# Optimization experiments

Measured on AMD Instinct MI355X. Metric: run time of the kernel, lower is better.

Reference implementation:

```python
import jax, jax.numpy as jnp
import numpy as np

B = 64
RX, RZ, RX_, RZ_ = 32, 16, 16, 8
TN = 1
STRIDE = 2
IN_DIM, OUT_DIM = 256, 512
KEY_DIM, H, ATTN_RATIO = 32, 8, 2
D = ATTN_RATIO * KEY_DIM            # per-head value dim = 64
DH = D * H                          # 512
NH_KD = KEY_DIM * H                 # 256
N = RX * RX + TN * RZ * RZ          # 1280 tokens (search + template)
N_ = RX_ * RX_ + TN * RZ_ * RZ_     # 320 subsampled query tokens
SCALE = KEY_DIM ** -0.5
EPS = 1e-5


def linear_bn(x, W, gamma, beta):
    # Linear (no bias) followed by BatchNorm1d in training mode over (B*N, C)
    y = jnp.einsum('bnc,oc->bno', x, W)
    m = y.mean(axis=(0, 1))
    v = y.var(axis=(0, 1))  # biased variance, as torch BN uses for normalization
    return (y - m) * jax.lax.rsqrt(v + EPS) * gamma + beta


def subsample(x):
    # stride-subsample the search-region tokens and each template's tokens
    b, n, c = x.shape
    parts = [x[:, :RX * RX].reshape(b, RX, RX, c)[:, ::STRIDE, ::STRIDE].reshape(b, -1, c)]
    for i in range(TN):
        s = RX * RX + i * RZ * RZ
        z = x[:, s:s + RZ * RZ].reshape(b, RZ, RZ, c)[:, ::STRIDE, ::STRIDE].reshape(b, -1, c)
        parts.append(z)
    return jnp.concatenate(parts, axis=1)


def setup_inputs() -> dict:
    key = jax.random.key(0)
    ks = jax.random.split(key, 4)
    return {
        'x': jax.random.normal(ks[0], (B, N, IN_DIM), dtype=jnp.float32),
        'W_kv': jax.random.normal(ks[1], (NH_KD + DH, IN_DIM), dtype=jnp.float32) * 0.02,
        'g_kv': jnp.ones((NH_KD + DH,), jnp.float32),
        'b_kv': jnp.zeros((NH_KD + DH,), jnp.float32),
        'W_q': jax.random.normal(ks[2], (NH_KD, IN_DIM), dtype=jnp.float32) * 0.02,
        'g_q': jnp.ones((NH_KD,), jnp.float32),
        'b_q': jnp.zeros((NH_KD,), jnp.float32),
        'W_p': jax.random.normal(ks[3], (OUT_DIM, DH), dtype=jnp.float32) * 0.02,
        'g_p': jnp.ones((OUT_DIM,), jnp.float32),
        'b_p': jnp.zeros((OUT_DIM,), jnp.float32),
    }


def reference(x, W_kv, g_kv, b_kv, W_q, g_q, b_q, W_p, g_p, b_p):
    b = x.shape[0]
    # fused KV projection + BN, then split into per-head K and V
    kv = linear_bn(x, W_kv, g_kv, b_kv).reshape(b, N, H, KEY_DIM + D)
    k = kv[..., :KEY_DIM].transpose(0, 2, 1, 3)   # [B,H,N,key_dim]
    v = kv[..., KEY_DIM:].transpose(0, 2, 1, 3)   # [B,H,N,d]
    # Q: subsample tokens, then Linear_BN
    q = linear_bn(subsample(x), W_q, g_q, b_q).reshape(b, N_, H, KEY_DIM).transpose(0, 2, 1, 3)
    attn = jax.nn.softmax(jnp.einsum('bhqd,bhkd->bhqk', q, k) * SCALE, axis=-1)
    o = jnp.einsum('bhqk,bhkd->bhqd', attn, v).transpose(0, 2, 1, 3).reshape(b, N_, DH)
    return linear_bn(jax.nn.hard_swish(o), W_p, g_p, b_p)
```

## Files before the change

kernel.cpp:

```cpp
#include <hip/hip_runtime.h>
#include <hip/hip_bf16.h>
#include <math.h>

#define EPSF 1e-5f
#define SCALEF 0.17677669529663687f
#define LOG2E 1.4426950408889634f

typedef unsigned short u16;
typedef unsigned int u32;
typedef __attribute__((ext_vector_type(8))) short bf16x8;
typedef __attribute__((ext_vector_type(4))) float f32x4;

__device__ __forceinline__ float b2f(u16 u) {
    union { unsigned int i; float f; } v; v.i = ((unsigned int)u) << 16; return v.f;
}
__device__ __forceinline__ u16 f2b(float f) {
    union { float f; unsigned int i; } v; v.f = f;
    unsigned int x = v.i;
    return (u16)((x + 0x7fffu + ((x >> 16) & 1u)) >> 16);
}
__device__ __forceinline__ float fexp2(float x) {
#if __has_builtin(__builtin_amdgcn_exp2f)
    return __builtin_amdgcn_exp2f(x);
#else
    return exp2f(x);
#endif
}
__device__ __forceinline__ u32 cvtpk_bf16(float lo, float hi) {
    u32 r;
    asm("v_cvt_pk_bf16_f32 %0, %1, %2" : "=v"(r) : "v"(lo), "v"(hi));
    return r;
}

__global__ void convert_f32_bf16(const float* __restrict__ src, u16* __restrict__ dst, int n4) {
    int i = blockIdx.x * 256 + threadIdx.x;
    if (i >= n4) return;
    float4 v = ((const float4*)src)[i];
    ushort4 o;
    o.x = f2b(v.x); o.y = f2b(v.y); o.z = f2b(v.z); o.w = f2b(v.w);
    ((ushort4*)dst)[i] = o;
}

__global__ void convert_wkv_perm(const float* __restrict__ W, u16* __restrict__ out) {
    int r = blockIdx.x, cl = threadIdx.x;
    int src = (r < 256) ? ((r >> 5) * 96 + (r & 31))
                        : (((r - 256) >> 6) * 96 + 32 + ((r - 256) & 63));
    out[r * 256 + cl] = f2b(W[src * 256 + cl]);
}

__global__ void gather_sub_bf16(const u16* __restrict__ xb, u16* __restrict__ xsub, int n8) {
    int i = blockIdx.x * 256 + threadIdx.x;
    if (i >= n8) return;
    int e = i << 3;
    int row = e >> 8;
    int col = e & 255;
    int b = row / 320;
    int t = row - b * 320;
    int n;
    if (t < 256) n = ((t >> 4) << 6) + ((t & 15) << 1);
    else { int tt = t - 256; n = 1024 + ((tt >> 3) << 5) + ((tt & 7) << 1); }
    *(int4*)(xsub + e) = *(const int4*)(xb + ((size_t)(b * 1280 + n)) * 256 + col);
}

template<int MODE, int NT, int KC>
__global__ __launch_bounds__(64) void gemm1w(const u16* __restrict__ A, const u16* __restrict__ Bw,
                                             void* __restrict__ Cv, void* __restrict__ C2v,
                                             int N, float* __restrict__ sums) {
    const int lane = threadIdx.x;
    const int quad = lane >> 4, lc = lane & 15;
    const int id = blockIdx.x;
    const int xcd = id & 7;
    const int l = id >> 3;
    const int mchunk = (int)(gridDim.x >> 3) / NT;
    const int m_t = xcd * mchunk + l / NT;
    const int n_t = l % NT;
    const int m0 = m_t * 64, n0 = n_t * 64;

    const u16* Ap = A  + (size_t)(m0 + lc) * KC + quad * 8;
    const u16* Bp = Bw + (size_t)(n0 + lc) * KC + quad * 8;

    f32x4 acc[4][4];
#pragma unroll
    for (int i = 0; i < 4; ++i)
#pragma unroll
        for (int j = 0; j < 4; ++j) acc[i][j] = (f32x4){0.f, 0.f, 0.f, 0.f};

#pragma unroll 2
    for (int k0 = 0; k0 < KC; k0 += 32) {
        bf16x8 af[4], bfr[4];
#pragma unroll
        for (int mi = 0; mi < 4; ++mi) af[mi]  = *(const bf16x8*)(Ap + (size_t)(mi * 16) * KC + k0);
#pragma unroll
        for (int ni = 0; ni < 4; ++ni) bfr[ni] = *(const bf16x8*)(Bp + (size_t)(ni * 16) * KC + k0);
#pragma unroll
        for (int mi = 0; mi < 4; ++mi)
#pragma unroll
            for (int ni = 0; ni < 4; ++ni)
                acc[mi][ni] = __builtin_amdgcn_mfma_f32_16x16x32_bf16(af[mi], bfr[ni], acc[mi][ni], 0, 0, 0);
    }

    float ps[4], ps2[4];
#pragma unroll
    for (int ni = 0; ni < 4; ++ni) { ps[ni] = 0.f; ps2[ni] = 0.f; }
#pragma unroll
    for (int mi = 0; mi < 4; ++mi)
#pragma unroll
        for (int ni = 0; ni < 4; ++ni)
#pragma unroll
            for (int r = 0; r < 4; ++r) {
                float v = acc[mi][ni][r];
                ps[ni] += v; ps2[ni] += v * v;
            }
#pragma unroll
    for (int ni = 0; ni < 4; ++ni) {
        ps[ni]  += __shfl_xor(ps[ni], 16);  ps[ni]  += __shfl_xor(ps[ni], 32);
        ps2[ni] += __shfl_xor(ps2[ni], 16); ps2[ni] += __shfl_xor(ps2[ni], 32);
    }
    if (quad == 0) {
        int rep = m_t & 7;
#pragma unroll
        for (int ni = 0; ni < 4; ++ni) {
            int c = n0 + ni * 16 + lc;
            atomicAdd(&sums[(rep * 2 + 0) * N + c], ps[ni]);
            atomicAdd(&sums[(rep * 2 + 1) * N + c], ps2[ni]);
        }
    }

    if (MODE == 0 || MODE == 1) {
#pragma unroll
        for (int mi = 0; mi < 4; ++mi)
#pragma unroll
            for (int ni = 0; ni < 4; ++ni)
#pragma unroll
                for (int r = 0; r < 4; ++r) {
                    int row = m0 + mi * 16 + quad * 4 + r;
                    int cn  = n0 + ni * 16 + lc;
                    float v = acc[mi][ni][r];
                    if (MODE == 1) ((float*)Cv)[(size_t)row * N + cn] = v;
                    else           ((u16*)Cv)[(size_t)row * N + cn] = f2b(v);
                }
    } else if (n0 < 256) {
        u16* Kr = (u16*)Cv;
#pragma unroll
        for (int mi = 0; mi < 4; ++mi)
#pragma unroll
            for (int r = 0; r < 4; ++r) {
                int t = m0 + mi * 16 + quad * 4 + r;
                int kk = t & 31;
                int pr = (t & ~31) + ((kk & 4) << 2) + ((kk >> 3) << 2) + (kk & 3);
#pragma unroll
                for (int ni = 0; ni < 4; ++ni) {
                    int c = n0 + ni * 16 + lc;
                    Kr[(size_t)pr * 256 + c] = f2b(acc[mi][ni][r]);
                }
            }
    } else {
        u16* Vt = (u16*)C2v;
#pragma unroll
        for (int mi = 0; mi < 4; ++mi)
#pragma unroll
            for (int ni = 0; ni < 4; ++ni) {
                int cp = n0 - 256 + ni * 16 + lc;
                int t0 = m0 + mi * 16 + quad * 4;
                uint2 w;
                w.x = cvtpk_bf16(acc[mi][ni][0], acc[mi][ni][1]);
                w.y = cvtpk_bf16(acc[mi][ni][2], acc[mi][ni][3]);
                *(uint2*)(Vt + (size_t)cp * 81920 + t0) = w;
            }
    }
}

__global__ void finalize_bn(const float* __restrict__ sum2, const float* __restrict__ g,
                            const float* __restrict__ beta, int cols, float inv_n, float scale,
                            float* __restrict__ AB, int kvperm) {
    int c = blockIdx.x * 256 + threadIdx.x;
    if (c >= cols) return;
    float s = 0.f, s2 = 0.f;
#pragma unroll
    for (int r = 0; r < 8; ++r) {
        s  += sum2[(r * 2 + 0) * cols + c];
        s2 += sum2[(r * 2 + 1) * cols + c];
    }
    int src = c;
    if (kvperm) {
        src = (c < 256) ? ((c >> 5) * 96 + (c & 31))
                        : (((c - 256) >> 6) * 96 + 32 + ((c - 256) & 63));
    }
    float m = s * inv_n;
    float var = s2 * inv_n - m * m;
    float a = g[src] * rsqrtf(var + EPSF) * scale;
    AB[c] = a;
    AB[cols + c] = beta[src] * scale - m * a;
}

__global__ __launch_bounds__(256, 2) void attn_kernel5(const u16* __restrict__ Kr, const u16* __restrict__ Vt,
                                                       const u16* __restrict__ q_raw,
                                                       const float* __restrict__ ABq,
                                                       const float* __restrict__ ABkv,
                                                       u16* __restrict__ o_act) {
    const int tid = threadIdx.x;
    const int wave = tid >> 6, lane = tid & 63;
    const int quad = lane >> 4, lc = lane & 15;
    const int h = blockIdx.x, b = blockIdx.y;

    float qa[8], qb[8];
#pragma unroll
    for (int j = 0; j < 8; ++j) {
        int c = h * 32 + quad * 8 + j;
        float ak = ABkv[c];
        qa[j] = ABq[c] * ak;
        qb[j] = ABq[256 + c] * ak;
    }
    bf16x8 qf[5];
#pragma unroll
    for (int j = 0; j < 5; ++j) {
        const u16* qs = q_raw + ((size_t)(b * 320 + j * 64 + wave * 16 + lc)) * 256 + h * 32 + quad * 8;
        union { int4 v; u16 u[8]; } ld; ld.v = *(const int4*)qs;
        union { bf16x8 v; u16 u[8]; } st;
#pragma unroll
        for (int jj = 0; jj < 8; ++jj) st.u[jj] = f2b(b2f(ld.u[jj]) * qa[jj] + qb[jj]);
        qf[j] = st.v;
    }

    const u16* Kp = Kr + (size_t)b * 1280 * 256 + (size_t)lc * 256 + h * 32 + quad * 8;
    const u16* Vp = Vt + ((size_t)(h * 64 + lc)) * 81920 + b * 1280 + quad * 8;

    f32x4 acc[5][4];
#pragma unroll
    for (int j = 0; j < 5; ++j)
#pragma unroll
        for (int i = 0; i < 4; ++i) acc[j][i] = (f32x4){0.f, 0.f, 0.f, 0.f};
    float lsum[5];
#pragma unroll
    for (int j = 0; j < 5; ++j) lsum[j] = 0.f;

    const f32x4 z = (f32x4){0.f, 0.f, 0.f, 0.f};
    for (int kc = 0; kc < 1280; kc += 32) {
        bf16x8 kfA = *(const bf16x8*)(Kp + (size_t)kc * 256);
        bf16x8 kfB = *(const bf16x8*)(Kp + (size_t)(kc + 16) * 256);
        bf16x8 vf0 = *(const bf16x8*)(Vp + kc);
        bf16x8 vf1 = *(const bf16x8*)(Vp + (size_t)16 * 81920 + kc);
        bf16x8 vf2 = *(const bf16x8*)(Vp + (size_t)32 * 81920 + kc);
        bf16x8 vf3 = *(const bf16x8*)(Vp + (size_t)48 * 81920 + kc);
        f32x4 s0[5], s1[5];
#pragma unroll
        for (int j = 0; j < 5; ++j) {
            s0[j] = __builtin_amdgcn_mfma_f32_16x16x32_bf16(kfA, qf[j], z, 0, 0, 0);
            s1[j] = __builtin_amdgcn_mfma_f32_16x16x32_bf16(kfB, qf[j], z, 0, 0, 0);
        }
#pragma unroll
        for (int j = 0; j < 5; ++j) {
            float p0 = fexp2(s0[j][0]);
            float p1 = fexp2(s0[j][1]);
            float p2 = fexp2(s0[j][2]);
            float p3 = fexp2(s0[j][3]);
            float p4 = fexp2(s1[j][0]);
            float p5 = fexp2(s1[j][1]);
            float p6 = fexp2(s1[j][2]);
            float p7 = fexp2(s1[j][3]);
            lsum[j] += ((p0 + p1) + (p2 + p3)) + ((p4 + p5) + (p6 + p7));
            union { u32 w[4]; bf16x8 v; } pf;
            pf.w[0] = cvtpk_bf16(p0, p1);
            pf.w[1] = cvtpk_bf16(p2, p3);
            pf.w[2] = cvtpk_bf16(p4, p5);
            pf.w[3] = cvtpk_bf16(p6, p7);
            acc[j][0] = __builtin_amdgcn_mfma_f32_16x16x32_bf16(vf0, pf.v, acc[j][0], 0, 0, 0);
            acc[j][1] = __builtin_amdgcn_mfma_f32_16x16x32_bf16(vf1, pf.v, acc[j][1], 0, 0, 0);
            acc[j][2] = __builtin_amdgcn_mfma_f32_16x16x32_bf16(vf2, pf.v, acc[j][2], 0, 0, 0);
            acc[j][3] = __builtin_amdgcn_mfma_f32_16x16x32_bf16(vf3, pf.v, acc[j][3], 0, 0, 0);
        }
    }
    float av[16], bv[16];
#pragma unroll
    for (int t = 0; t < 16; ++t) {
        int cv = 256 + h * 64 + (t >> 2) * 16 + quad * 4 + (t & 3);
        av[t] = ABkv[cv];
        bv[t] = ABkv[768 + cv];
    }
#pragma unroll
    for (int j = 0; j < 5; ++j) {
        float l = lsum[j];
        l += __shfl_xor(l, 16);
        l += __shfl_xor(l, 32);
        float inv = 1.f / l;
        int qrow = b * 320 + j * 64 + wave * 16 + lc;
        u16* dst = o_act + (size_t)qrow * 512 + h * 64 + quad * 4;
#pragma unroll
        for (int nt = 0; nt < 4; ++nt) {
            ushort4 st;
#pragma unroll
            for (int r = 0; r < 4; ++r) {
                float o = av[nt * 4 + r] * (acc[j][nt][r] * inv) + bv[nt * 4 + r];
                float hs = o * fminf(fmaxf(o + 3.f, 0.f), 6.f) * (1.f / 6.f);
                ((u16*)&st)[r] = f2b(hs);
            }
            *(ushort4*)(dst + nt * 16) = st;
        }
    }
}

__global__ void bn_apply_out(const float* __restrict__ praw, const float* __restrict__ ABp,
                             float* __restrict__ out, int n4) {
    int i = blockIdx.x * 256 + threadIdx.x;
    if (i >= n4) return;
    int e = i << 2;
    int c = e & 511;
    float4 v = ((const float4*)praw)[i];
    float4 o;
    o.x = v.x * ABp[c]     + ABp[512 + c];
    o.y = v.y * ABp[c + 1] + ABp[512 + c + 1];
    o.z = v.z * ABp[c + 2] + ABp[512 + c + 2];
    o.w = v.w * ABp[c + 3] + ABp[512 + c + 3];
    ((float4*)out)[i] = o;
}

extern "C" void kernel_launch(void* const* d_in, const int* in_sizes, int n_in,
                              void* d_out, int out_size, void* d_ws, size_t ws_size,
                              hipStream_t stream) {
    const float* x   = (const float*)d_in[0];
    const float* Wkv = (const float*)d_in[1];
    const float* gkv = (const float*)d_in[2];
    const float* bkv = (const float*)d_in[3];
    const float* Wq  = (const float*)d_in[4];
    const float* gq  = (const float*)d_in[5];
    const float* bq  = (const float*)d_in[6];
    const float* Wp  = (const float*)d_in[7];
    const float* gp  = (const float*)d_in[8];
    const float* bp  = (const float*)d_in[9];
    float* out = (float*)d_out;

    char* ws = (char*)d_ws;
    size_t off = 0;
    auto alloc = [&](size_t bytes) -> void* {
        void* p = ws + off;
        off += (bytes + 255) & ~(size_t)255;
        return p;
    };
    void*  slot1  = alloc(81920ull * 256 * 2);
    u16*   x_b    = (u16*)slot1;
    float* p_raw  = (float*)slot1;
    u16*   K_raw  = (u16*)alloc(81920ull * 256 * 2);
    u16*   Vt_raw = (u16*)alloc(512ull * 81920 * 2);
    u16*   q_raw  = (u16*)alloc(20480ull * 256 * 2);
    void*  slot2  = alloc(20480ull * 512 * 2);
    u16*   xsub_b = (u16*)slot2;
    u16*   o_act  = (u16*)slot2;
    u16*   Wkv_b  = (u16*)alloc(768ull * 256 * 2);
    u16*   Wq_b   = (u16*)alloc(256ull * 256 * 2);
    u16*   Wp_b   = (u16*)alloc(512ull * 512 * 2);
    float* sums_kv = (float*)alloc(8 * 2 * 768 * sizeof(float));
    float* sums_q  = (float*)alloc(8 * 2 * 256 * sizeof(float));
    float* sums_p  = (float*)alloc(8 * 2 * 512 * sizeof(float));
    float* ABkv = (float*)alloc(1536 * sizeof(float));
    float* ABq  = (float*)alloc(512 * sizeof(float));
    float* ABp  = (float*)alloc(1024 * sizeof(float));

    dim3 blk(256);
    hipMemsetAsync(sums_kv, 0, 8 * 2 * (768 + 256 + 512) * sizeof(float), stream);

    convert_f32_bf16<<<20480, blk, 0, stream>>>(x,   x_b,   5242880);
    convert_wkv_perm<<<768,   blk, 0, stream>>>(Wkv, Wkv_b);
    convert_f32_bf16<<<64,    blk, 0, stream>>>(Wq,  Wq_b,  16384);
    convert_f32_bf16<<<256,   blk, 0, stream>>>(Wp,  Wp_b,  65536);
    gather_sub_bf16<<<2560,   blk, 0, stream>>>(x_b, xsub_b, 655360);

    gemm1w<2, 12, 256><<<15360, 64, 0, stream>>>(x_b,    Wkv_b, K_raw, Vt_raw, 768, sums_kv);
    gemm1w<0, 4,  256><<<1280,  64, 0, stream>>>(xsub_b, Wq_b,  q_raw, nullptr, 256, sums_q);

    finalize_bn<<<3, blk, 0, stream>>>(sums_kv, gkv, bkv, 768, 1.f / 81920.f, 1.f, ABkv, 1);
    finalize_bn<<<1, blk, 0, stream>>>(sums_q,  gq,  bq,  256, 1.f / 20480.f, SCALEF * LOG2E, ABq, 0);

    attn_kernel5<<<dim3(8, 64), blk, 0, stream>>>(K_raw, Vt_raw, q_raw, ABq, ABkv, o_act);

    gemm1w<1, 8, 512><<<2560, 64, 0, stream>>>(o_act, Wp_b, p_raw, nullptr, 512, sums_p);
    finalize_bn<<<2, blk, 0, stream>>>(sums_p, gp, bp, 512, 1.f / 20480.f, 1.f, ABp, 0);

    bn_apply_out<<<10240, blk, 0, stream>>>(p_raw, ABp, out, 2621440);
}
```

Before: 431.1 us.

## Replace single-wave GEMM with 4-wave 128x128 tiles staging A in LDS

```diff
diff --git a/kernel.cpp b/kernel.cpp
--- a/kernel.cpp
+++ b/kernel.cpp
@@ -30,6 +30,11 @@
     u32 r;
     asm("v_cvt_pk_bf16_f32 %0, %1, %2" : "=v"(r) : "v"(lo), "v"(hi));
     return r;
+}
+__device__ __forceinline__ void gload_lds16(const u16* __restrict__ g, u16* l) {
+    __builtin_amdgcn_global_load_lds(
+        (const __attribute__((address_space(1))) void*)g,
+        (__attribute__((address_space(3))) void*)l, 16, 0, 0);
 }
 
 __global__ void convert_f32_bf16(const float* __restrict__ src, u16* __restrict__ dst, int n4) {
@@ -63,21 +68,24 @@
 }
 
 template<int MODE, int NT, int KC>
-__global__ __launch_bounds__(64) void gemm1w(const u16* __restrict__ A, const u16* __restrict__ Bw,
-                                             void* __restrict__ Cv, void* __restrict__ C2v,
-                                             int N, float* __restrict__ sums) {
-    const int lane = threadIdx.x;
+__global__ __launch_bounds__(256) void gemm_ls(const u16* __restrict__ A, const u16* __restrict__ Bw,
+                                               void* __restrict__ Cv, void* __restrict__ C2v,
+                                               int N, float* __restrict__ sums) {
+    __shared__ u16 As[128 * 256];
+    const int tid = threadIdx.x;
+    const int wave = tid >> 6, lane = tid & 63;
     const int quad = lane >> 4, lc = lane & 15;
+    const int wr = wave >> 1, wc = wave & 1;
     const int id = blockIdx.x;
-    const int xcd = id & 7;
-    const int l = id >> 3;
-    const int mchunk = (int)(gridDim.x >> 3) / NT;
+    const int xcd = id & 7, l = id >> 3;
+    const int mchunk = ((int)gridDim.x >> 3) / NT;
     const int m_t = xcd * mchunk + l / NT;
-    const int n_t = l % NT;
-    const int m0 = m_t * 64, n0 = n_t * 64;
-
-    const u16* Ap = A  + (size_t)(m0 + lc) * KC + quad * 8;
-    const u16* Bp = Bw + (size_t)(n0 + lc) * KC + quad * 8;
+    const int n_t = l - (l / NT) * NT;
+    const int m0 = m_t * 128, n0 = n_t * 128;
+
+    const int r_in = lane >> 5;
+    const int g_l  = lane & 31;
+    const u16* Bp = Bw + (size_t)(n0 + wc * 64 + lc) * KC + quad * 8;
 
     f32x4 acc[4][4];
 #pragma unroll
@@ -85,18 +93,35 @@
 #pragma unroll
         for (int j = 0; j < 4; ++j) acc[i][j] = (f32x4){0.f, 0.f, 0.f, 0.f};
 
-#pragma unroll 2
-    for (int k0 = 0; k0 < KC; k0 += 32) {
-        bf16x8 af[4], bfr[4];
-#pragma unroll
-        for (int mi = 0; mi < 4; ++mi) af[mi]  = *(const bf16x8*)(Ap + (size_t)(mi * 16) * KC + k0);
-#pragma unroll
-        for (int ni = 0; ni < 4; ++ni) bfr[ni] = *(const bf16x8*)(Bp + (size_t)(ni * 16) * KC + k0);
-#pragma unroll
-        for (int mi = 0; mi < 4; ++mi)
+    for (int kb = 0; kb < KC; kb += 256) {
+        if (kb) __syncthreads();
+#pragma unroll
+        for (int s = 0; s < 16; ++s) {
+            int Rb = wave * 32 + s * 2;
+            int R  = Rb + r_in;
+            int col = ((g_l ^ (R & 7)) << 3) + kb;
+            gload_lds16(A + (size_t)(m0 + R) * KC + col, &As[Rb * 256]);
+        }
+        asm volatile("s_waitcnt vmcnt(0)" ::: "memory");
+        __syncthreads();
+#pragma unroll
+        for (int t = 0; t < 8; ++t) {
+            bf16x8 af[4], bfr[4];
+#pragma unroll
+            for (int mi = 0; mi < 4; ++mi) {
+                int R = wr * 64 + mi * 16 + lc;
+                int g = (t * 4 + quad) ^ (R & 7);
+                af[mi] = *(const bf16x8*)&As[R * 256 + g * 8];
+            }
 #pragma unroll
             for (int ni = 0; ni < 4; ++ni)
-                acc[mi][ni] = __builtin_amdgcn_mfma_f32_16x16x32_bf16(af[mi], bfr[ni], acc[mi][ni], 0, 0, 0);
+                bfr[ni] = *(const bf16x8*)(Bp + (size_t)(ni * 16) * KC + kb + t * 32);
+#pragma unroll
+            for (int mi = 0; mi < 4; ++mi)
+#pragma unroll
+                for (int ni = 0; ni < 4; ++ni)
+                    acc[mi][ni] = __builtin_amdgcn_mfma_f32_16x16x32_bf16(af[mi], bfr[ni], acc[mi][ni], 0, 0, 0);
+        }
     }
 
     float ps[4], ps2[4];
@@ -120,7 +145,7 @@
         int rep = m_t & 7;
 #pragma unroll
         for (int ni = 0; ni < 4; ++ni) {
-            int c = n0 + ni * 16 + lc;
+            int c = n0 + wc * 64 + ni * 16 + lc;
             atomicAdd(&sums[(rep * 2 + 0) * N + c], ps[ni]);
             atomicAdd(&sums[(rep * 2 + 1) * N + c], ps2[ni]);
         }
@@ -133,8 +158,8 @@
             for (int ni = 0; ni < 4; ++ni)
 #pragma unroll
                 for (int r = 0; r < 4; ++r) {
-                    int row = m0 + mi * 16 + quad * 4 + r;
-                    int cn  = n0 + ni * 16 + lc;
+                    int row = m0 + wr * 64 + mi * 16 + quad * 4 + r;
+                    int cn  = n0 + wc * 64 + ni * 16 + lc;
                     float v = acc[mi][ni][r];
                     if (MODE == 1) ((float*)Cv)[(size_t)row * N + cn] = v;
                     else           ((u16*)Cv)[(size_t)row * N + cn] = f2b(v);
@@ -145,12 +170,12 @@
         for (int mi = 0; mi < 4; ++mi)
 #pragma unroll
             for (int r = 0; r < 4; ++r) {
-                int t = m0 + mi * 16 + quad * 4 + r;
+                int t = m0 + wr * 64 + mi * 16 + quad * 4 + r;
                 int kk = t & 31;
                 int pr = (t & ~31) + ((kk & 4) << 2) + ((kk >> 3) << 2) + (kk & 3);
 #pragma unroll
                 for (int ni = 0; ni < 4; ++ni) {
-                    int c = n0 + ni * 16 + lc;
+                    int c = n0 + wc * 64 + ni * 16 + lc;
                     Kr[(size_t)pr * 256 + c] = f2b(acc[mi][ni][r]);
                 }
             }
@@ -160,8 +185,8 @@
         for (int mi = 0; mi < 4; ++mi)
 #pragma unroll
             for (int ni = 0; ni < 4; ++ni) {
-                int cp = n0 - 256 + ni * 16 + lc;
-                int t0 = m0 + mi * 16 + quad * 4;
+                int cp = n0 - 256 + wc * 64 + ni * 16 + lc;
+                int t0 = m0 + wr * 64 + mi * 16 + quad * 4;
                 uint2 w;
                 w.x = cvtpk_bf16(acc[mi][ni][0], acc[mi][ni][1]);
                 w.y = cvtpk_bf16(acc[mi][ni][2], acc[mi][ni][3]);
@@ -364,15 +389,15 @@
     convert_f32_bf16<<<256,   blk, 0, stream>>>(Wp,  Wp_b,  65536);
     gather_sub_bf16<<<2560,   blk, 0, stream>>>(x_b, xsub_b, 655360);
 
-    gemm1w<2, 12, 256><<<15360, 64, 0, stream>>>(x_b,    Wkv_b, K_raw, Vt_raw, 768, sums_kv);
-    gemm1w<0, 4,  256><<<1280,  64, 0, stream>>>(xsub_b, Wq_b,  q_raw, nullptr, 256, sums_q);
+    gemm_ls<2, 6, 256><<<3840, blk, 0, stream>>>(x_b,    Wkv_b, K_raw, Vt_raw, 768, sums_kv);
+    gemm_ls<0, 2, 256><<<320,  blk, 0, stream>>>(xsub_b, Wq_b,  q_raw, nullptr, 256, sums_q);
 
     finalize_bn<<<3, blk, 0, stream>>>(sums_kv, gkv, bkv, 768, 1.f / 81920.f, 1.f, ABkv, 1);
     finalize_bn<<<1, blk, 0, stream>>>(sums_q,  gq,  bq,  256, 1.f / 20480.f, SCALEF * LOG2E, ABq, 0);
 
     attn_kernel5<<<dim3(8, 64), blk, 0, stream>>>(K_raw, Vt_raw, q_raw, ABq, ABkv, o_act);
 
-    gemm1w<1, 8, 512><<<2560, 64, 0, stream>>>(o_act, Wp_b, p_raw, nullptr, 512, sums_p);
+    gemm_ls<1, 4, 512><<<640, blk, 0, stream>>>(o_act, Wp_b, p_raw, nullptr, 512, sums_p);
     finalize_bn<<<2, blk, 0, stream>>>(sums_p, gp, bp, 512, 1.f / 20480.f, 1.f, ABp, 0);
 
     bn_apply_out<<<10240, blk, 0, stream>>>(p_raw, ABp, out, 2621440);
```

Result: faster. 380.4 us (-11.8%).
